# Performance work log

Measured on AMD Instinct MI355X. Metric: run time of the kernel, lower is better.

The kernel has to match this reference:

```python
import jax, jax.numpy as jnp
import numpy as np

N_NODES = 1_000_000
N_GRAPHS = 4096
EPS = 1e-16


def setup_inputs() -> dict:
    key = jax.random.key(0)
    ks = jax.random.split(key, 9)
    x = jax.random.normal(ks[0], (N_NODES, 64), dtype=jnp.float32)
    node_batch = jnp.sort(jax.random.randint(ks[1], (N_NODES,), 0, N_GRAPHS)).astype(jnp.int64)
    global_attr = jax.random.normal(ks[2], (N_GRAPHS, 3), dtype=jnp.float32)
    s3, s128, s64 = 1.0 / np.sqrt(3.0), 1.0 / np.sqrt(128.0), 1.0 / np.sqrt(64.0)
    Wg = jax.random.uniform(ks[3], (3, 64), minval=-s3, maxval=s3, dtype=jnp.float32)
    bg = jax.random.uniform(ks[4], (64,), minval=-s3, maxval=s3, dtype=jnp.float32)
    Wn = jax.random.uniform(ks[5], (128, 64), minval=-s128, maxval=s128, dtype=jnp.float32)
    bn = jax.random.uniform(ks[6], (64,), minval=-s128, maxval=s128, dtype=jnp.float32)
    Wa = jax.random.uniform(ks[7], (64, 1), minval=-s64, maxval=s64, dtype=jnp.float32)
    ba = jax.random.uniform(ks[8], (1,), minval=-s64, maxval=s64, dtype=jnp.float32)
    return {"x": x, "node_batch": node_batch, "global_attr": global_attr,
            "Wg": Wg, "bg": bg, "Wn": Wn, "bn": bn, "Wa": Wa, "ba": ba}


def _segment_softmax(scores, seg, num_segments):
    # scores: [N]; seg: [N] int ids. Numerically stable per-segment softmax.
    m = jax.ops.segment_max(scores, seg, num_segments=num_segments)
    e = jnp.exp(scores - m[seg])
    denom = jax.ops.segment_sum(e, seg, num_segments=num_segments)
    return e / (denom[seg] + EPS)


def reference(x, node_batch, global_attr, Wg, bg, Wn, bn, Wa, ba):
    seg = node_batch.astype(jnp.int32)
    g = global_attr @ Wg + bg                    # [B, 64]
    graph_embed = g[seg]                         # repeat_interleave broadcast -> [N, 64]
    chunk = jnp.concatenate([x, graph_embed], axis=-1)   # [N, 128]
    h = jax.nn.softplus(chunk @ Wn + bn)         # [N, 64]
    s = (h @ Wa + ba)[:, 0]                      # [N]
    w = _segment_softmax(s, seg, N_GRAPHS)       # [N]
    return w[:, None]                            # [N, 1]
```

## Files before the change

kernel.cpp:

```cpp
#include <hip/hip_runtime.h>
#include <hip/hip_bf16.h>
#include <stdint.h>

#define N_NODES_C 1000000
#define N_GRAPHS_C 4096
#define SPAN 96

typedef __attribute__((ext_vector_type(8))) __bf16 bf16x8;
typedef __attribute__((ext_vector_type(2))) __bf16 bf16x2;
typedef __attribute__((ext_vector_type(4))) float f32x4;

__device__ __forceinline__ unsigned short f2bf(float f) {
    union { float f; unsigned int u; } v; v.f = f;
    unsigned int r = v.u + 0x7FFFu + ((v.u >> 16) & 1u);
    return (unsigned short)(r >> 16);
}
__device__ __forceinline__ unsigned int pack2(float a, float b) {
#if __has_builtin(__builtin_amdgcn_cvt_pk_bf16_f32)
    bf16x2 r = __builtin_amdgcn_cvt_pk_bf16_f32(a, b);
    union { bf16x2 v; unsigned int u; } cv; cv.v = r;
    return cv.u;
#else
    return (unsigned int)f2bf(a) | ((unsigned int)f2bf(b) << 16);
#endif
}

__global__ __launch_bounds__(256) void stage0_kernel(
    const float* __restrict__ ga, const float* __restrict__ Wg,
    const float* __restrict__ bg, const float* __restrict__ Wn,
    const float* __restrict__ bn,
    float* __restrict__ c, unsigned short* __restrict__ BT,
    float* __restrict__ denom)
{
    __shared__ float Wns[64 * 64];
    __shared__ float gs[4][64];
    int t = threadIdx.x;
#pragma unroll
    for (int i = 0; i < 4; ++i)
        ((float4*)Wns)[t + i * 256] = ((const float4*)(Wn + 64 * 64))[t + i * 256];
    if (blockIdx.x == 0) {
#pragma unroll
        for (int i = 0; i < 16; ++i) {
            int flat = t * 16 + i;
            int n = flat >> 6, k = flat & 63;
            BT[flat] = f2bf(Wn[k * 64 + n]);
        }
    }
    int gl = t >> 6, j = t & 63;
    int b = blockIdx.x * 4 + gl;
    float acc = bg[j];
#pragma unroll
    for (int m = 0; m < 3; ++m) acc += ga[b * 3 + m] * Wg[m * 64 + j];
    gs[gl][j] = acc;
    __syncthreads();
    float cj = bn[j];
#pragma unroll 16
    for (int k = 0; k < 64; ++k) cj += gs[gl][k] * Wns[k * 64 + j];
    c[b * 64 + j] = cj;
    if (j == 0) denom[b] = 0.0f;
}

__global__ __launch_bounds__(256, 4) void node_kernel(
    const float* __restrict__ x, const int* __restrict__ nb,
    const float* __restrict__ c, const unsigned short* __restrict__ BT,
    const float* __restrict__ Wa, const float* __restrict__ ba,
    float* __restrict__ e, float* __restrict__ denom)
{
    __shared__ float part[SPAN];
    int t = threadIdx.x;
    int wave = t >> 6, lane = t & 63;
    int quad = lane >> 4, l15 = lane & 15;
    int blockbase = blockIdx.x * 64;
    int base = blockbase + wave * 16;
    bool is64 = nb[N_NODES_C - 1] < 1024;

    if (t < SPAN) part[t] = 0.0f;

    const float4* xp = (const float4*)(x + (long)(base + l15) * 64);
    float4 v0 = xp[quad * 2];
    float4 v1 = xp[quad * 2 + 1];
    float4 v2 = xp[8 + quad * 2];
    float4 v3 = xp[8 + quad * 2 + 1];

    int g0 = is64 ? nb[2L * blockbase] : nb[blockbase];
    int segown = is64 ? nb[2L * (base + l15)] : nb[base + l15];
    int sg0 = __shfl(segown, quad * 4 + 0, 64);
    int sg1 = __shfl(segown, quad * 4 + 1, 64);
    int sg2 = __shfl(segown, quad * 4 + 2, 64);
    int sg3 = __shfl(segown, quad * 4 + 3, 64);

    bf16x8 b0[4], b1[4];
#pragma unroll
    for (int nt = 0; nt < 4; ++nt) {
        b0[nt] = *(const bf16x8*)&BT[(nt * 16 + l15) * 64 + quad * 8];
        b1[nt] = *(const bf16x8*)&BT[(nt * 16 + l15) * 64 + quad * 8 + 32];
    }
    float wa[4];
    float bav = ba[0];
#pragma unroll
    for (int nt = 0; nt < 4; ++nt) wa[nt] = Wa[nt * 16 + l15];

    union { bf16x8 v; unsigned int u[4]; } A0, A1;
    A0.u[0] = pack2(v0.x, v0.y); A0.u[1] = pack2(v0.z, v0.w);
    A0.u[2] = pack2(v1.x, v1.y); A0.u[3] = pack2(v1.z, v1.w);
    A1.u[0] = pack2(v2.x, v2.y); A1.u[1] = pack2(v2.z, v2.w);
    A1.u[2] = pack2(v3.x, v3.y); A1.u[3] = pack2(v3.z, v3.w);

    __syncthreads();

    f32x4 acc[4];
#pragma unroll
    for (int nt = 0; nt < 4; ++nt) {
        acc[nt] = (f32x4){0.f, 0.f, 0.f, 0.f};
        acc[nt] = __builtin_amdgcn_mfma_f32_16x16x32_bf16(A0.v, b0[nt], acc[nt], 0, 0, 0);
        acc[nt] = __builtin_amdgcn_mfma_f32_16x16x32_bf16(A1.v, b1[nt], acc[nt], 0, 0, 0);
    }

    int r0 = base + quad * 4;
    bool uni = (sg0 == sg3);
    float sp0 = 0.f, sp1 = 0.f, sp2 = 0.f, sp3 = 0.f;
#pragma unroll
    for (int nt = 0; nt < 4; ++nt) {
        int col = nt * 16 + l15;
        float c0, c1, c2, c3;
        if (uni) { c0 = c[sg0 * 64 + col]; c1 = c0; c2 = c0; c3 = c0; }
        else {
            c0 = c[sg0 * 64 + col]; c1 = c[sg1 * 64 + col];
            c2 = c[sg2 * 64 + col]; c3 = c[sg3 * 64 + col];
        }
        float y0 = acc[nt].x + c0, y1 = acc[nt].y + c1;
        float y2 = acc[nt].z + c2, y3 = acc[nt].w + c3;
        sp0 += __logf(1.f + __expf(y0)) * wa[nt];
        sp1 += __logf(1.f + __expf(y1)) * wa[nt];
        sp2 += __logf(1.f + __expf(y2)) * wa[nt];
        sp3 += __logf(1.f + __expf(y3)) * wa[nt];
    }
#pragma unroll
    for (int off = 1; off < 16; off <<= 1) {
        sp0 += __shfl_xor(sp0, off, 64);
        sp1 += __shfl_xor(sp1, off, 64);
        sp2 += __shfl_xor(sp2, off, 64);
        sp3 += __shfl_xor(sp3, off, 64);
    }
    float e0 = __expf(sp0 + bav), e1 = __expf(sp1 + bav);
    float e2 = __expf(sp2 + bav), e3 = __expf(sp3 + bav);
    if (l15 == 0) {
        *(float4*)&e[r0] = make_float4(e0, e1, e2, e3);
        float s = e0; int cur = sg0;
        if (sg1 == cur) s += e1; else {
            unsigned int i0 = cur - g0;
            if (i0 < SPAN) atomicAdd(&part[i0], s); else atomicAdd(&denom[cur], s);
            cur = sg1; s = e1;
        }
        if (sg2 == cur) s += e2; else {
            unsigned int i0 = cur - g0;
            if (i0 < SPAN) atomicAdd(&part[i0], s); else atomicAdd(&denom[cur], s);
            cur = sg2; s = e2;
        }
        if (sg3 == cur) s += e3; else {
            unsigned int i0 = cur - g0;
            if (i0 < SPAN) atomicAdd(&part[i0], s); else atomicAdd(&denom[cur], s);
            cur = sg3; s = e3;
        }
        unsigned int i0 = cur - g0;
        if (i0 < SPAN) atomicAdd(&part[i0], s); else atomicAdd(&denom[cur], s);
    }
    __syncthreads();
    if (t < SPAN) {
        float v = part[t];
        if (v != 0.0f) atomicAdd(&denom[g0 + t], v);
    }
}

__global__ __launch_bounds__(256) void fin_kernel(
    const float* __restrict__ e, const int* __restrict__ nb,
    const float* __restrict__ denom, float* __restrict__ out)
{
    long node0 = (long)(blockIdx.x * 256 + threadIdx.x) * 4;
    if (node0 >= N_NODES_C) return;
    bool is64 = nb[N_NODES_C - 1] < 1024;
    float4 ev = *(const float4*)&e[node0];
    int s0, s1, s2, s3;
    if (is64) {
        int4 a = *(const int4*)&nb[2 * node0];
        int4 b = *(const int4*)&nb[2 * node0 + 4];
        s0 = a.x; s1 = a.z; s2 = b.x; s3 = b.z;
    } else {
        int4 a = *(const int4*)&nb[node0];
        s0 = a.x; s1 = a.y; s2 = a.z; s3 = a.w;
    }
    float4 w;
    w.x = ev.x / denom[s0];
    w.y = ev.y / denom[s1];
    w.z = ev.z / denom[s2];
    w.w = ev.w / denom[s3];
    *(float4*)&out[node0] = w;
}

extern "C" void kernel_launch(void* const* d_in, const int* in_sizes, int n_in,
                              void* d_out, int out_size, void* d_ws, size_t ws_size,
                              hipStream_t stream) {
    const float* x  = (const float*)d_in[0];
    const int*   nb = (const int*)d_in[1];
    const float* ga = (const float*)d_in[2];
    const float* Wg = (const float*)d_in[3];
    const float* bg = (const float*)d_in[4];
    const float* Wn = (const float*)d_in[5];
    const float* bn = (const float*)d_in[6];
    const float* Wa = (const float*)d_in[7];
    const float* ba = (const float*)d_in[8];

    char* ws = (char*)d_ws;
    float* e            = (float*)(ws);
    float* c            = (float*)(ws + 4194304);
    unsigned short* BT  = (unsigned short*)(ws + 4194304 + 1048576);
    float* denom        = (float*)(ws + 4194304 + 1048576 + 8192);

    hipLaunchKernelGGL(stage0_kernel, dim3(N_GRAPHS_C / 4), dim3(256), 0, stream,
                       ga, Wg, bg, Wn, bn, c, BT, denom);
    hipLaunchKernelGGL(node_kernel, dim3(N_NODES_C / 64), dim3(256), 0, stream,
                       x, nb, c, BT, Wa, ba, e, denom);
    hipLaunchKernelGGL(fin_kernel, dim3((N_NODES_C / 4 + 255) / 256), dim3(256), 0, stream,
                       e, nb, denom, (float*)d_out);
}
```

Before: 377.0 us.

## Fold graph-embedding precompute into node kernel and normalise per graph

Removes the separate stage0 kernel. The graph-embedding term is refactored into a 3x64 matrix plus a bias vector, computed per block from Wn staged in LDS. Each node block now also builds the bf16 B fragments itself and processes four 64-node tiles. Exponentials are written straight to the output, and the finish kernel does a per-graph binary search, block reduction and in-place scaling, replacing the global and shared atomics and the workspace buffers. The trade-off is that every block reloads 32KB of Wn and repeats the small matmul, and the finish kernel pays for binary searches and two passes over each segment.

```diff
diff --git a/kernel.cpp b/kernel.cpp
--- a/kernel.cpp
+++ b/kernel.cpp
@@ -4,7 +4,6 @@
 
 #define N_NODES_C 1000000
 #define N_GRAPHS_C 4096
-#define SPAN 96
 
 typedef __attribute__((ext_vector_type(8))) __bf16 bf16x8;
 typedef __attribute__((ext_vector_type(2))) __bf16 bf16x2;
@@ -25,176 +24,180 @@
 #endif
 }
 
-__global__ __launch_bounds__(256) void stage0_kernel(
+__global__ __launch_bounds__(256, 4) void node_kernel(
+    const float* __restrict__ x, const int* __restrict__ nb,
     const float* __restrict__ ga, const float* __restrict__ Wg,
     const float* __restrict__ bg, const float* __restrict__ Wn,
-    const float* __restrict__ bn,
-    float* __restrict__ c, unsigned short* __restrict__ BT,
-    float* __restrict__ denom)
+    const float* __restrict__ bn, const float* __restrict__ Wa,
+    const float* __restrict__ ba, float* __restrict__ out)
 {
-    __shared__ float Wns[64 * 64];
-    __shared__ float gs[4][64];
-    int t = threadIdx.x;
-#pragma unroll
-    for (int i = 0; i < 4; ++i)
-        ((float4*)Wns)[t + i * 256] = ((const float4*)(Wn + 64 * 64))[t + i * 256];
-    if (blockIdx.x == 0) {
-#pragma unroll
-        for (int i = 0; i < 16; ++i) {
-            int flat = t * 16 + i;
-            int n = flat >> 6, k = flat & 63;
-            BT[flat] = f2bf(Wn[k * 64 + n]);
-        }
-    }
-    int gl = t >> 6, j = t & 63;
-    int b = blockIdx.x * 4 + gl;
-    float acc = bg[j];
-#pragma unroll
-    for (int m = 0; m < 3; ++m) acc += ga[b * 3 + m] * Wg[m * 64 + j];
-    gs[gl][j] = acc;
-    __syncthreads();
-    float cj = bn[j];
-#pragma unroll 16
-    for (int k = 0; k < 64; ++k) cj += gs[gl][k] * Wns[k * 64 + j];
-    c[b * 64 + j] = cj;
-    if (j == 0) denom[b] = 0.0f;
-}
-
-__global__ __launch_bounds__(256, 4) void node_kernel(
-    const float* __restrict__ x, const int* __restrict__ nb,
-    const float* __restrict__ c, const unsigned short* __restrict__ BT,
-    const float* __restrict__ Wa, const float* __restrict__ ba,
-    float* __restrict__ e, float* __restrict__ denom)
-{
-    __shared__ float part[SPAN];
+    __shared__ float Wns[128 * 64];
+    __shared__ float Ms[4][64];
+
     int t = threadIdx.x;
     int wave = t >> 6, lane = t & 63;
     int quad = lane >> 4, l15 = lane & 15;
-    int blockbase = blockIdx.x * 64;
-    int base = blockbase + wave * 16;
+    int blockbase = blockIdx.x * 256;
+    int avail = N_NODES_C - blockbase;
+    int nIter = (avail >= 256) ? 4 : (avail >> 6);
     bool is64 = nb[N_NODES_C - 1] < 1024;
 
-    if (t < SPAN) part[t] = 0.0f;
-
-    const float4* xp = (const float4*)(x + (long)(base + l15) * 64);
-    float4 v0 = xp[quad * 2];
-    float4 v1 = xp[quad * 2 + 1];
-    float4 v2 = xp[8 + quad * 2];
-    float4 v3 = xp[8 + quad * 2 + 1];
-
-    int g0 = is64 ? nb[2L * blockbase] : nb[blockbase];
-    int segown = is64 ? nb[2L * (base + l15)] : nb[base + l15];
-    int sg0 = __shfl(segown, quad * 4 + 0, 64);
-    int sg1 = __shfl(segown, quad * 4 + 1, 64);
-    int sg2 = __shfl(segown, quad * 4 + 2, 64);
-    int sg3 = __shfl(segown, quad * 4 + 3, 64);
+#pragma unroll
+    for (int i = 0; i < 8; ++i)
+        ((float4*)Wns)[t + i * 256] = ((const float4*)Wn)[t + i * 256];
+    __syncthreads();
+
+    {
+        int m = t >> 6, j = t & 63;
+        float accv;
+        if (m == 3) {
+            accv = bn[j];
+#pragma unroll 16
+            for (int k = 0; k < 64; ++k) accv += bg[k] * Wns[(64 + k) * 64 + j];
+        } else {
+            accv = 0.f;
+#pragma unroll 16
+            for (int k = 0; k < 64; ++k) accv += Wg[m * 64 + k] * Wns[(64 + k) * 64 + j];
+        }
+        Ms[m][j] = accv;
+    }
+    __syncthreads();
 
     bf16x8 b0[4], b1[4];
 #pragma unroll
     for (int nt = 0; nt < 4; ++nt) {
-        b0[nt] = *(const bf16x8*)&BT[(nt * 16 + l15) * 64 + quad * 8];
-        b1[nt] = *(const bf16x8*)&BT[(nt * 16 + l15) * 64 + quad * 8 + 32];
-    }
-    float wa[4];
+        int n = nt * 16 + l15;
+        union { bf16x8 v; unsigned int u[4]; } B;
+#pragma unroll
+        for (int p = 0; p < 4; ++p)
+            B.u[p] = pack2(Wns[(quad * 8 + 2 * p) * 64 + n],
+                           Wns[(quad * 8 + 2 * p + 1) * 64 + n]);
+        b0[nt] = B.v;
+#pragma unroll
+        for (int p = 0; p < 4; ++p)
+            B.u[p] = pack2(Wns[(32 + quad * 8 + 2 * p) * 64 + n],
+                           Wns[(32 + quad * 8 + 2 * p + 1) * 64 + n]);
+        b1[nt] = B.v;
+    }
+
+    float Mreg[4][3], C0r[4], wa[4];
+#pragma unroll
+    for (int nt = 0; nt < 4; ++nt) {
+        int n = nt * 16 + l15;
+        Mreg[nt][0] = Ms[0][n]; Mreg[nt][1] = Ms[1][n]; Mreg[nt][2] = Ms[2][n];
+        C0r[nt] = Ms[3][n];
+        wa[nt] = Wa[n];
+    }
     float bav = ba[0];
-#pragma unroll
-    for (int nt = 0; nt < 4; ++nt) wa[nt] = Wa[nt * 16 + l15];
-
-    union { bf16x8 v; unsigned int u[4]; } A0, A1;
-    A0.u[0] = pack2(v0.x, v0.y); A0.u[1] = pack2(v0.z, v0.w);
-    A0.u[2] = pack2(v1.x, v1.y); A0.u[3] = pack2(v1.z, v1.w);
-    A1.u[0] = pack2(v2.x, v2.y); A1.u[1] = pack2(v2.z, v2.w);
-    A1.u[2] = pack2(v3.x, v3.y); A1.u[3] = pack2(v3.z, v3.w);
-
-    __syncthreads();
-
-    f32x4 acc[4];
-#pragma unroll
-    for (int nt = 0; nt < 4; ++nt) {
-        acc[nt] = (f32x4){0.f, 0.f, 0.f, 0.f};
-        acc[nt] = __builtin_amdgcn_mfma_f32_16x16x32_bf16(A0.v, b0[nt], acc[nt], 0, 0, 0);
-        acc[nt] = __builtin_amdgcn_mfma_f32_16x16x32_bf16(A1.v, b1[nt], acc[nt], 0, 0, 0);
-    }
-
-    int r0 = base + quad * 4;
-    bool uni = (sg0 == sg3);
-    float sp0 = 0.f, sp1 = 0.f, sp2 = 0.f, sp3 = 0.f;
-#pragma unroll
-    for (int nt = 0; nt < 4; ++nt) {
-        int col = nt * 16 + l15;
-        float c0, c1, c2, c3;
-        if (uni) { c0 = c[sg0 * 64 + col]; c1 = c0; c2 = c0; c3 = c0; }
-        else {
-            c0 = c[sg0 * 64 + col]; c1 = c[sg1 * 64 + col];
-            c2 = c[sg2 * 64 + col]; c3 = c[sg3 * 64 + col];
-        }
-        float y0 = acc[nt].x + c0, y1 = acc[nt].y + c1;
-        float y2 = acc[nt].z + c2, y3 = acc[nt].w + c3;
-        sp0 += __logf(1.f + __expf(y0)) * wa[nt];
-        sp1 += __logf(1.f + __expf(y1)) * wa[nt];
-        sp2 += __logf(1.f + __expf(y2)) * wa[nt];
-        sp3 += __logf(1.f + __expf(y3)) * wa[nt];
-    }
-#pragma unroll
-    for (int off = 1; off < 16; off <<= 1) {
-        sp0 += __shfl_xor(sp0, off, 64);
-        sp1 += __shfl_xor(sp1, off, 64);
-        sp2 += __shfl_xor(sp2, off, 64);
-        sp3 += __shfl_xor(sp3, off, 64);
-    }
-    float e0 = __expf(sp0 + bav), e1 = __expf(sp1 + bav);
-    float e2 = __expf(sp2 + bav), e3 = __expf(sp3 + bav);
-    if (l15 == 0) {
-        *(float4*)&e[r0] = make_float4(e0, e1, e2, e3);
-        float s = e0; int cur = sg0;
-        if (sg1 == cur) s += e1; else {
-            unsigned int i0 = cur - g0;
-            if (i0 < SPAN) atomicAdd(&part[i0], s); else atomicAdd(&denom[cur], s);
-            cur = sg1; s = e1;
-        }
-        if (sg2 == cur) s += e2; else {
-            unsigned int i0 = cur - g0;
-            if (i0 < SPAN) atomicAdd(&part[i0], s); else atomicAdd(&denom[cur], s);
-            cur = sg2; s = e2;
-        }
-        if (sg3 == cur) s += e3; else {
-            unsigned int i0 = cur - g0;
-            if (i0 < SPAN) atomicAdd(&part[i0], s); else atomicAdd(&denom[cur], s);
-            cur = sg3; s = e3;
-        }
-        unsigned int i0 = cur - g0;
-        if (i0 < SPAN) atomicAdd(&part[i0], s); else atomicAdd(&denom[cur], s);
-    }
-    __syncthreads();
-    if (t < SPAN) {
-        float v = part[t];
-        if (v != 0.0f) atomicAdd(&denom[g0 + t], v);
+
+    for (int it = 0; it < nIter; ++it) {
+        int base = blockbase + it * 64 + wave * 16;
+
+        const float4* xp = (const float4*)(x + (long)(base + l15) * 64);
+        float4 v0 = xp[quad * 2];
+        float4 v1 = xp[quad * 2 + 1];
+        float4 v2 = xp[8 + quad * 2];
+        float4 v3 = xp[8 + quad * 2 + 1];
+
+        int segown = is64 ? nb[2L * (base + l15)] : nb[base + l15];
+        int sg0 = __shfl(segown, quad * 4 + 0, 64);
+        int sg1 = __shfl(segown, quad * 4 + 1, 64);
+        int sg2 = __shfl(segown, quad * 4 + 2, 64);
+        int sg3 = __shfl(segown, quad * 4 + 3, 64);
+
+        union { bf16x8 v; unsigned int u[4]; } A0, A1;
+        A0.u[0] = pack2(v0.x, v0.y); A0.u[1] = pack2(v0.z, v0.w);
+        A0.u[2] = pack2(v1.x, v1.y); A0.u[3] = pack2(v1.z, v1.w);
+        A1.u[0] = pack2(v2.x, v2.y); A1.u[1] = pack2(v2.z, v2.w);
+        A1.u[2] = pack2(v3.x, v3.y); A1.u[3] = pack2(v3.z, v3.w);
+
+        f32x4 acc[4];
+#pragma unroll
+        for (int nt = 0; nt < 4; ++nt) {
+            acc[nt] = (f32x4){0.f, 0.f, 0.f, 0.f};
+            acc[nt] = __builtin_amdgcn_mfma_f32_16x16x32_bf16(A0.v, b0[nt], acc[nt], 0, 0, 0);
+            acc[nt] = __builtin_amdgcn_mfma_f32_16x16x32_bf16(A1.v, b1[nt], acc[nt], 0, 0, 0);
+        }
+
+        bool uni = (sg0 == sg3);
+        float a00 = ga[sg0 * 3], a01 = ga[sg0 * 3 + 1], a02 = ga[sg0 * 3 + 2];
+        float a10, a11, a12, a20, a21, a22, a30, a31, a32;
+        if (uni) {
+            a10 = a00; a11 = a01; a12 = a02;
+            a20 = a00; a21 = a01; a22 = a02;
+            a30 = a00; a31 = a01; a32 = a02;
+        } else {
+            a10 = ga[sg1 * 3]; a11 = ga[sg1 * 3 + 1]; a12 = ga[sg1 * 3 + 2];
+            a20 = ga[sg2 * 3]; a21 = ga[sg2 * 3 + 1]; a22 = ga[sg2 * 3 + 2];
+            a30 = ga[sg3 * 3]; a31 = ga[sg3 * 3 + 1]; a32 = ga[sg3 * 3 + 2];
+        }
+
+        float sp0 = 0.f, sp1 = 0.f, sp2 = 0.f, sp3 = 0.f;
+#pragma unroll
+        for (int nt = 0; nt < 4; ++nt) {
+            float m0 = Mreg[nt][0], m1 = Mreg[nt][1], m2 = Mreg[nt][2], cc = C0r[nt];
+            float y0 = acc[nt].x + cc + a00 * m0 + a01 * m1 + a02 * m2;
+            float y1 = acc[nt].y + cc + a10 * m0 + a11 * m1 + a12 * m2;
+            float y2 = acc[nt].z + cc + a20 * m0 + a21 * m1 + a22 * m2;
+            float y3 = acc[nt].w + cc + a30 * m0 + a31 * m1 + a32 * m2;
+            sp0 += __logf(1.f + __expf(y0)) * wa[nt];
+            sp1 += __logf(1.f + __expf(y1)) * wa[nt];
+            sp2 += __logf(1.f + __expf(y2)) * wa[nt];
+            sp3 += __logf(1.f + __expf(y3)) * wa[nt];
+        }
+#pragma unroll
+        for (int off = 1; off < 16; off <<= 1) {
+            sp0 += __shfl_xor(sp0, off, 64);
+            sp1 += __shfl_xor(sp1, off, 64);
+            sp2 += __shfl_xor(sp2, off, 64);
+            sp3 += __shfl_xor(sp3, off, 64);
+        }
+        if (l15 == 0) {
+            int r0 = base + quad * 4;
+            *(float4*)&out[r0] = make_float4(__expf(sp0 + bav), __expf(sp1 + bav),
+                                             __expf(sp2 + bav), __expf(sp3 + bav));
+        }
     }
 }
 
 __global__ __launch_bounds__(256) void fin_kernel(
-    const float* __restrict__ e, const int* __restrict__ nb,
-    const float* __restrict__ denom, float* __restrict__ out)
+    const int* __restrict__ nb, float* __restrict__ out)
 {
-    long node0 = (long)(blockIdx.x * 256 + threadIdx.x) * 4;
-    if (node0 >= N_NODES_C) return;
+    int g = blockIdx.x;
     bool is64 = nb[N_NODES_C - 1] < 1024;
-    float4 ev = *(const float4*)&e[node0];
-    int s0, s1, s2, s3;
-    if (is64) {
-        int4 a = *(const int4*)&nb[2 * node0];
-        int4 b = *(const int4*)&nb[2 * node0 + 4];
-        s0 = a.x; s1 = a.z; s2 = b.x; s3 = b.z;
-    } else {
-        int4 a = *(const int4*)&nb[node0];
-        s0 = a.x; s1 = a.y; s2 = a.z; s3 = a.w;
-    }
-    float4 w;
-    w.x = ev.x / denom[s0];
-    w.y = ev.y / denom[s1];
-    w.z = ev.z / denom[s2];
-    w.w = ev.w / denom[s3];
-    *(float4*)&out[node0] = w;
+    int start, end;
+    {
+        int lo = 0, hi = N_NODES_C;
+        while (lo < hi) {
+            int mid = (lo + hi) >> 1;
+            int v = is64 ? nb[2L * mid] : nb[mid];
+            if (v < g) lo = mid + 1; else hi = mid;
+        }
+        start = lo;
+        lo = start; hi = N_NODES_C;
+        while (lo < hi) {
+            int mid = (lo + hi) >> 1;
+            int v = is64 ? nb[2L * mid] : nb[mid];
+            if (v < g + 1) lo = mid + 1; else hi = mid;
+        }
+        end = lo;
+    }
+    if (end <= start) return;
+
+    int t = threadIdx.x;
+    float s = 0.f;
+    for (int i = start + t; i < end; i += 256) s += out[i];
+#pragma unroll
+    for (int off = 32; off; off >>= 1) s += __shfl_down(s, off, 64);
+    __shared__ float wsum[4];
+    __shared__ float dsh;
+    int lane = t & 63, w = t >> 6;
+    if (lane == 0) wsum[w] = s;
+    __syncthreads();
+    if (t == 0) dsh = wsum[0] + wsum[1] + wsum[2] + wsum[3];
+    __syncthreads();
+    float inv = 1.0f / dsh;
+    for (int i = start + t; i < end; i += 256) out[i] *= inv;
 }
 
 extern "C" void kernel_launch(void* const* d_in, const int* in_sizes, int n_in,
@@ -209,17 +212,11 @@
     const float* bn = (const float*)d_in[6];
     const float* Wa = (const float*)d_in[7];
     const float* ba = (const float*)d_in[8];
-
-    char* ws = (char*)d_ws;
-    float* e            = (float*)(ws);
-    float* c            = (float*)(ws + 4194304);
-    unsigned short* BT  = (unsigned short*)(ws + 4194304 + 1048576);
-    float* denom        = (float*)(ws + 4194304 + 1048576 + 8192);
-
-    hipLaunchKernelGGL(stage0_kernel, dim3(N_GRAPHS_C / 4), dim3(256), 0, stream,
-                       ga, Wg, bg, Wn, bn, c, BT, denom);
-    hipLaunchKernelGGL(node_kernel, dim3(N_NODES_C / 64), dim3(256), 0, stream,
-                       x, nb, c, BT, Wa, ba, e, denom);
-    hipLaunchKernelGGL(fin_kernel, dim3((N_NODES_C / 4 + 255) / 256), dim3(256), 0, stream,
-                       e, nb, denom, (float*)d_out);
-}
+    float* outp = (float*)d_out;
+    (void)d_ws; (void)ws_size;
+
+    hipLaunchKernelGGL(node_kernel, dim3((N_NODES_C + 255) / 256), dim3(256), 0, stream,
+                       x, nb, ga, Wg, bg, Wn, bn, Wa, ba, outp);
+    hipLaunchKernelGGL(fin_kernel, dim3(N_GRAPHS_C), dim3(256), 0, stream,
+                       nb, outp);
+}
```

New measurement: 396.8 us. 5.3% more time.

## Make node kernel persistent with register prefetch and fold Wg into Wn

Applied to the files above, without the earlier changes.

The node kernel now runs on a fixed grid of 1024 blocks. Each block walks a contiguous range of 64-node tiles, and each wave prefetches the next chunk's x rows and segment ids into registers while it computes the current chunk. This spreads the per-block setup (B fragments, Wa, shared partial flush) over many tiles and overlaps global loads with MFMA and softplus work. Stage0 is changed to first compute Wg·Wn and bg·Wn+bn per block, so each graph's bias row becomes a 3-term combination; this cuts the stage0 grid by 16x. The cost is more register pressure from the prefetch buffers and less parallelism than the old one-tile-per-block launch.

```diff
diff --git a/kernel.cpp b/kernel.cpp
--- a/kernel.cpp
+++ b/kernel.cpp
@@ -4,6 +4,8 @@
 
 #define N_NODES_C 1000000
 #define N_GRAPHS_C 4096
+#define NTILES 15625
+#define NODE_GRID 1024
 #define SPAN 96
 
 typedef __attribute__((ext_vector_type(8))) __bf16 bf16x8;
@@ -33,7 +35,7 @@
     float* __restrict__ denom)
 {
     __shared__ float Wns[64 * 64];
-    __shared__ float gs[4][64];
+    __shared__ float Ms[4][64];
     int t = threadIdx.x;
 #pragma unroll
     for (int i = 0; i < 4; ++i)
@@ -46,18 +48,30 @@
             BT[flat] = f2bf(Wn[k * 64 + n]);
         }
     }
+    __syncthreads();
+    {
+        int m = t >> 6, j = t & 63;
+        float accv;
+        if (m == 3) {
+            accv = bn[j];
+#pragma unroll 16
+            for (int k = 0; k < 64; ++k) accv += bg[k] * Wns[k * 64 + j];
+        } else {
+            accv = 0.f;
+#pragma unroll 16
+            for (int k = 0; k < 64; ++k) accv += Wg[m * 64 + k] * Wns[k * 64 + j];
+        }
+        Ms[m][j] = accv;
+    }
+    __syncthreads();
     int gl = t >> 6, j = t & 63;
-    int b = blockIdx.x * 4 + gl;
-    float acc = bg[j];
-#pragma unroll
-    for (int m = 0; m < 3; ++m) acc += ga[b * 3 + m] * Wg[m * 64 + j];
-    gs[gl][j] = acc;
-    __syncthreads();
-    float cj = bn[j];
-#pragma unroll 16
-    for (int k = 0; k < 64; ++k) cj += gs[gl][k] * Wns[k * 64 + j];
-    c[b * 64 + j] = cj;
-    if (j == 0) denom[b] = 0.0f;
+    float m0 = Ms[0][j], m1 = Ms[1][j], m2 = Ms[2][j], c0v = Ms[3][j];
+#pragma unroll
+    for (int i = 0; i < 16; ++i) {
+        int b = blockIdx.x * 64 + i * 4 + gl;
+        c[b * 64 + j] = c0v + ga[b * 3] * m0 + ga[b * 3 + 1] * m1 + ga[b * 3 + 2] * m2;
+    }
+    if (t < 64) denom[blockIdx.x * 64 + t] = 0.0f;
 }
 
 __global__ __launch_bounds__(256, 4) void node_kernel(
@@ -70,24 +84,18 @@
     int t = threadIdx.x;
     int wave = t >> 6, lane = t & 63;
     int quad = lane >> 4, l15 = lane & 15;
-    int blockbase = blockIdx.x * 64;
-    int base = blockbase + wave * 16;
+
+    int b = blockIdx.x;
+    int q = NTILES / NODE_GRID, r = NTILES % NODE_GRID;
+    int tstart = b * q + (b < r ? b : r);
+    int tcount = q + (b < r ? 1 : 0);
+    int node0 = tstart * 64;
+    int chunks = tcount * 4;
+
     bool is64 = nb[N_NODES_C - 1] < 1024;
+    int g0 = is64 ? nb[2L * node0] : nb[node0];
 
     if (t < SPAN) part[t] = 0.0f;
-
-    const float4* xp = (const float4*)(x + (long)(base + l15) * 64);
-    float4 v0 = xp[quad * 2];
-    float4 v1 = xp[quad * 2 + 1];
-    float4 v2 = xp[8 + quad * 2];
-    float4 v3 = xp[8 + quad * 2 + 1];
-
-    int g0 = is64 ? nb[2L * blockbase] : nb[blockbase];
-    int segown = is64 ? nb[2L * (base + l15)] : nb[base + l15];
-    int sg0 = __shfl(segown, quad * 4 + 0, 64);
-    int sg1 = __shfl(segown, quad * 4 + 1, 64);
-    int sg2 = __shfl(segown, quad * 4 + 2, 64);
-    int sg3 = __shfl(segown, quad * 4 + 3, 64);
 
     bf16x8 b0[4], b1[4];
 #pragma unroll
@@ -100,71 +108,107 @@
 #pragma unroll
     for (int nt = 0; nt < 4; ++nt) wa[nt] = Wa[nt * 16 + l15];
 
-    union { bf16x8 v; unsigned int u[4]; } A0, A1;
-    A0.u[0] = pack2(v0.x, v0.y); A0.u[1] = pack2(v0.z, v0.w);
-    A0.u[2] = pack2(v1.x, v1.y); A0.u[3] = pack2(v1.z, v1.w);
-    A1.u[0] = pack2(v2.x, v2.y); A1.u[1] = pack2(v2.z, v2.w);
-    A1.u[2] = pack2(v3.x, v3.y); A1.u[3] = pack2(v3.z, v3.w);
-
-    __syncthreads();
-
-    f32x4 acc[4];
-#pragma unroll
-    for (int nt = 0; nt < 4; ++nt) {
-        acc[nt] = (f32x4){0.f, 0.f, 0.f, 0.f};
-        acc[nt] = __builtin_amdgcn_mfma_f32_16x16x32_bf16(A0.v, b0[nt], acc[nt], 0, 0, 0);
-        acc[nt] = __builtin_amdgcn_mfma_f32_16x16x32_bf16(A1.v, b1[nt], acc[nt], 0, 0, 0);
-    }
-
-    int r0 = base + quad * 4;
-    bool uni = (sg0 == sg3);
-    float sp0 = 0.f, sp1 = 0.f, sp2 = 0.f, sp3 = 0.f;
-#pragma unroll
-    for (int nt = 0; nt < 4; ++nt) {
-        int col = nt * 16 + l15;
-        float c0, c1, c2, c3;
-        if (uni) { c0 = c[sg0 * 64 + col]; c1 = c0; c2 = c0; c3 = c0; }
-        else {
-            c0 = c[sg0 * 64 + col]; c1 = c[sg1 * 64 + col];
-            c2 = c[sg2 * 64 + col]; c3 = c[sg3 * 64 + col];
-        }
-        float y0 = acc[nt].x + c0, y1 = acc[nt].y + c1;
-        float y2 = acc[nt].z + c2, y3 = acc[nt].w + c3;
-        sp0 += __logf(1.f + __expf(y0)) * wa[nt];
-        sp1 += __logf(1.f + __expf(y1)) * wa[nt];
-        sp2 += __logf(1.f + __expf(y2)) * wa[nt];
-        sp3 += __logf(1.f + __expf(y3)) * wa[nt];
-    }
-#pragma unroll
-    for (int off = 1; off < 16; off <<= 1) {
-        sp0 += __shfl_xor(sp0, off, 64);
-        sp1 += __shfl_xor(sp1, off, 64);
-        sp2 += __shfl_xor(sp2, off, 64);
-        sp3 += __shfl_xor(sp3, off, 64);
-    }
-    float e0 = __expf(sp0 + bav), e1 = __expf(sp1 + bav);
-    float e2 = __expf(sp2 + bav), e3 = __expf(sp3 + bav);
-    if (l15 == 0) {
-        *(float4*)&e[r0] = make_float4(e0, e1, e2, e3);
-        float s = e0; int cur = sg0;
-        if (sg1 == cur) s += e1; else {
+    __syncthreads();
+
+    int j = wave;
+    float4 a0, a1, a2, a3; int segc = 0;
+    if (j < chunks) {
+        int base = node0 + j * 16;
+        const float4* xp = (const float4*)(x + (long)(base + l15) * 64);
+        a0 = xp[quad * 2];
+        a1 = xp[quad * 2 + 1];
+        a2 = xp[8 + quad * 2];
+        a3 = xp[8 + quad * 2 + 1];
+        segc = is64 ? nb[2L * (base + l15)] : nb[base + l15];
+    }
+    while (j < chunks) {
+        int jn = j + 4;
+        float4 n0, n1, n2, n3; int segn = 0;
+        if (jn < chunks) {
+            int nbase = node0 + jn * 16;
+            const float4* xp = (const float4*)(x + (long)(nbase + l15) * 64);
+            n0 = xp[quad * 2];
+            n1 = xp[quad * 2 + 1];
+            n2 = xp[8 + quad * 2];
+            n3 = xp[8 + quad * 2 + 1];
+            segn = is64 ? nb[2L * (nbase + l15)] : nb[nbase + l15];
+        } else {
+            n0 = n1 = n2 = n3 = make_float4(0.f, 0.f, 0.f, 0.f);
+        }
+
+        int base = node0 + j * 16;
+        int sg0 = __shfl(segc, quad * 4 + 0, 64);
+        int sg1 = __shfl(segc, quad * 4 + 1, 64);
+        int sg2 = __shfl(segc, quad * 4 + 2, 64);
+        int sg3 = __shfl(segc, quad * 4 + 3, 64);
+
+        union { bf16x8 v; unsigned int u[4]; } A0, A1;
+        A0.u[0] = pack2(a0.x, a0.y); A0.u[1] = pack2(a0.z, a0.w);
+        A0.u[2] = pack2(a1.x, a1.y); A0.u[3] = pack2(a1.z, a1.w);
+        A1.u[0] = pack2(a2.x, a2.y); A1.u[1] = pack2(a2.z, a2.w);
+        A1.u[2] = pack2(a3.x, a3.y); A1.u[3] = pack2(a3.z, a3.w);
+
+        f32x4 acc[4];
+#pragma unroll
+        for (int nt = 0; nt < 4; ++nt) {
+            acc[nt] = (f32x4){0.f, 0.f, 0.f, 0.f};
+            acc[nt] = __builtin_amdgcn_mfma_f32_16x16x32_bf16(A0.v, b0[nt], acc[nt], 0, 0, 0);
+            acc[nt] = __builtin_amdgcn_mfma_f32_16x16x32_bf16(A1.v, b1[nt], acc[nt], 0, 0, 0);
+        }
+
+        bool uni = (sg0 == sg3);
+        float sp0 = 0.f, sp1 = 0.f, sp2 = 0.f, sp3 = 0.f;
+#pragma unroll
+        for (int nt = 0; nt < 4; ++nt) {
+            int col = nt * 16 + l15;
+            float c0, c1, c2, c3;
+            if (uni) { c0 = c[sg0 * 64 + col]; c1 = c0; c2 = c0; c3 = c0; }
+            else {
+                c0 = c[sg0 * 64 + col]; c1 = c[sg1 * 64 + col];
+                c2 = c[sg2 * 64 + col]; c3 = c[sg3 * 64 + col];
+            }
+            float y0 = acc[nt].x + c0, y1 = acc[nt].y + c1;
+            float y2 = acc[nt].z + c2, y3 = acc[nt].w + c3;
+            sp0 += __logf(1.f + __expf(y0)) * wa[nt];
+            sp1 += __logf(1.f + __expf(y1)) * wa[nt];
+            sp2 += __logf(1.f + __expf(y2)) * wa[nt];
+            sp3 += __logf(1.f + __expf(y3)) * wa[nt];
+        }
+#pragma unroll
+        for (int off = 1; off < 16; off <<= 1) {
+            sp0 += __shfl_xor(sp0, off, 64);
+            sp1 += __shfl_xor(sp1, off, 64);
+            sp2 += __shfl_xor(sp2, off, 64);
+            sp3 += __shfl_xor(sp3, off, 64);
+        }
+        float e0 = __expf(sp0 + bav), e1 = __expf(sp1 + bav);
+        float e2 = __expf(sp2 + bav), e3 = __expf(sp3 + bav);
+        if (l15 == 0) {
+            *(float4*)&e[base + quad * 4] = make_float4(e0, e1, e2, e3);
+            float s = e0; int cur = sg0;
+            if (sg1 == cur) s += e1; else {
+                unsigned int i0 = cur - g0;
+                if (i0 < SPAN) atomicAdd(&part[i0], s); else atomicAdd(&denom[cur], s);
+                cur = sg1; s = e1;
+            }
+            if (sg2 == cur) s += e2; else {
+                unsigned int i0 = cur - g0;
+                if (i0 < SPAN) atomicAdd(&part[i0], s); else atomicAdd(&denom[cur], s);
+                cur = sg2; s = e2;
+            }
+            if (sg3 == cur) s += e3; else {
+                unsigned int i0 = cur - g0;
+                if (i0 < SPAN) atomicAdd(&part[i0], s); else atomicAdd(&denom[cur], s);
+                cur = sg3; s = e3;
+            }
             unsigned int i0 = cur - g0;
             if (i0 < SPAN) atomicAdd(&part[i0], s); else atomicAdd(&denom[cur], s);
-            cur = sg1; s = e1;
-        }
-        if (sg2 == cur) s += e2; else {
-            unsigned int i0 = cur - g0;
-            if (i0 < SPAN) atomicAdd(&part[i0], s); else atomicAdd(&denom[cur], s);
-            cur = sg2; s = e2;
-        }
-        if (sg3 == cur) s += e3; else {
-            unsigned int i0 = cur - g0;
-            if (i0 < SPAN) atomicAdd(&part[i0], s); else atomicAdd(&denom[cur], s);
-            cur = sg3; s = e3;
-        }
-        unsigned int i0 = cur - g0;
-        if (i0 < SPAN) atomicAdd(&part[i0], s); else atomicAdd(&denom[cur], s);
-    }
+        }
+
+        a0 = n0; a1 = n1; a2 = n2; a3 = n3; segc = segn;
+        j = jn;
+    }
+
     __syncthreads();
     if (t < SPAN) {
         float v = part[t];
@@ -216,9 +260,9 @@
     unsigned short* BT  = (unsigned short*)(ws + 4194304 + 1048576);
     float* denom        = (float*)(ws + 4194304 + 1048576 + 8192);
 
-    hipLaunchKernelGGL(stage0_kernel, dim3(N_GRAPHS_C / 4), dim3(256), 0, stream,
+    hipLaunchKernelGGL(stage0_kernel, dim3(N_GRAPHS_C / 64), dim3(256), 0, stream,
                        ga, Wg, bg, Wn, bn, c, BT, denom);
-    hipLaunchKernelGGL(node_kernel, dim3(N_NODES_C / 64), dim3(256), 0, stream,
+    hipLaunchKernelGGL(node_kernel, dim3(NODE_GRID), dim3(256), 0, stream,
                        x, nb, c, BT, Wa, ba, e, denom);
     hipLaunchKernelGGL(fin_kernel, dim3((N_NODES_C / 4 + 255) / 256), dim3(256), 0, stream,
                        e, nb, denom, (float*)d_out);
```

Measured after the change: 380.9 us. About the same (+1.0%).
